# Performance work log

Hardware: AMD Instinct MI355X
Metric: run time of the kernel (lower is better)

The kernel has to match this reference:

```python
import jax, jax.numpy as jnp
import numpy as np


def setup_inputs() -> dict:
    key = jax.random.key(0)
    k1, k2, k3, k4 = jax.random.split(key, 4)
    B, T, E, H = 16, 2048, 1024, 128
    x = jax.random.normal(k1, (B, T, E), dtype=jnp.float32)
    Wk = jax.random.normal(k2, (E, H), dtype=jnp.float32) * (E ** -0.5)
    Wq = jax.random.normal(k3, (E, H), dtype=jnp.float32) * (E ** -0.5)
    Wv = jax.random.normal(k4, (E, H), dtype=jnp.float32) * (E ** -0.5)
    return {"x": x, "Wk": Wk, "Wq": Wq, "Wv": Wv}


def reference(x, Wk, Wq, Wv):
    # x: [B,T,E]; Wk/Wq/Wv: [E,H]
    B, T, E = x.shape
    H = Wk.shape[1]
    k = jnp.einsum('bte,eh->bth', x, Wk)
    q = jnp.einsum('bte,eh->bth', x, Wq)
    v = jnp.einsum('bte,eh->bth', x, Wv)
    # scores [B,T,T]; original masks with -inf THEN scales (equivalent math)
    scores = jnp.einsum('bqh,bkh->bqk', q, k) * (H ** -0.5)
    causal = jnp.tril(jnp.ones((T, T), dtype=bool))
    scores = jnp.where(causal, scores, -jnp.inf)
    weights = jax.nn.softmax(scores, axis=-1)
    # dropout disabled (eval mode reference)
    return jnp.einsum('bqk,bkh->bqh', weights, v)
```

## Files before the change

### kernel.cpp

```cpp
#include <hip/hip_runtime.h>

#define B_ 16
#define T_ 2048
#define E_ 1024
#define H_ 128

typedef short bf16x8 __attribute__((ext_vector_type(8)));
typedef float f32x4 __attribute__((ext_vector_type(4)));
typedef unsigned short u16x4 __attribute__((ext_vector_type(4)));

static __device__ __forceinline__ unsigned short f2bf(float f) {
    unsigned int u = __float_as_uint(f);
    u += 0x7FFFu + ((u >> 16) & 1u);
    return (unsigned short)(u >> 16);
}
static __device__ __forceinline__ unsigned int pk2(unsigned short a, unsigned short b) {
    return (unsigned int)a | ((unsigned int)b << 16);
}
static __device__ __forceinline__ bf16x8 frag(uint4 v) {
    return __builtin_bit_cast(bf16x8, v);
}

__global__ __launch_bounds__(256) void wcvt_kernel(
    const float* __restrict__ w0, const float* __restrict__ w1,
    const float* __restrict__ w2, unsigned short* __restrict__ wt)
{
    int g   = blockIdx.x * 256 + threadIdx.x;
    int arr = g >> 14;
    int rem = g & 16383;
    int h   = rem >> 7;
    int e0  = (rem & 127) * 8;
    const float* src = (arr == 0) ? w0 : (arr == 1) ? w1 : w2;
    unsigned short b[8];
#pragma unroll
    for (int i = 0; i < 8; i++) b[i] = f2bf(src[(size_t)(e0 + i) * H_ + h]);
    uint4 o;
    o.x = pk2(b[0], b[1]); o.y = pk2(b[2], b[3]);
    o.z = pk2(b[4], b[5]); o.w = pk2(b[6], b[7]);
    size_t off = ((size_t)(e0 >> 5) * 384 + arr * 128 + h) * 32 + (e0 & 31);
    *(uint4*)&wt[off] = o;
}

__global__ __launch_bounds__(384, 3) void proj_kernel(
    const float* __restrict__ x,
    const unsigned short* __restrict__ wt,
    unsigned short* __restrict__ q_ws,
    unsigned short* __restrict__ k_ws,
    unsigned short* __restrict__ vt_ws)
{
    const int m0    = blockIdx.x * 128;
    const int nbase = blockIdx.y * 192;
    __shared__ __align__(16) unsigned short Xs[128][40];
    __shared__ __align__(16) unsigned short Wl[192][40];

    const int tid  = threadIdx.x;
    const int lane = tid & 63;
    const int w    = tid >> 6;
    const int quad = lane >> 4;
    const int lm   = lane & 15;
    const int rw   = (w & 1) * 64;
    const int cw   = (w >> 1) * 64;

    const f32x4 z4 = {0.f, 0.f, 0.f, 0.f};
    f32x4 acc[4][4];
#pragma unroll
    for (int i = 0; i < 4; i++)
#pragma unroll
        for (int j = 0; j < 4; j++) acc[i][j] = z4;

    for (int kb = 0; kb < 32; kb++) {
        const int k0 = kb * 32;
        __syncthreads();
#pragma unroll
        for (int j = 0; j < 2; j++) {
            int idx = j * 384 + tid;
            if (idx < 512) {
                int row = idx >> 2, c = (idx & 3) * 8;
                const float* xp = x + (size_t)(m0 + row) * E_ + k0 + c;
                float4 a = *(const float4*)xp;
                float4 b = *(const float4*)(xp + 4);
                uint4 u;
                u.x = pk2(f2bf(a.x), f2bf(a.y));
                u.y = pk2(f2bf(a.z), f2bf(a.w));
                u.z = pk2(f2bf(b.x), f2bf(b.y));
                u.w = pk2(f2bf(b.z), f2bf(b.w));
                *(uint4*)&Xs[row][c] = u;
            }
        }
#pragma unroll
        for (int j = 0; j < 2; j++) {
            int fl = (j * 384 + tid) * 8;
            int nl = fl >> 5, kk = fl & 31;
            *(uint4*)&Wl[nl][kk] =
                *(const uint4*)&wt[((size_t)kb * 384 + nbase + nl) * 32 + kk];
        }
        __syncthreads();

        bf16x8 a[4], b[4];
#pragma unroll
        for (int am = 0; am < 4; am++)
            a[am] = frag(*(const uint4*)&Xs[rw + am * 16 + lm][quad * 8]);
#pragma unroll
        for (int bn = 0; bn < 4; bn++)
            b[bn] = frag(*(const uint4*)&Wl[cw + bn * 16 + lm][quad * 8]);
#pragma unroll
        for (int am = 0; am < 4; am++)
#pragma unroll
            for (int bn = 0; bn < 4; bn++)
                acc[am][bn] = __builtin_amdgcn_mfma_f32_16x16x32_bf16(
                    a[am], b[bn], acc[am][bn], 0, 0, 0);
    }

    const int bb = m0 >> 11;
    const int t0 = m0 & 2047;
#pragma unroll
    for (int am = 0; am < 4; am++)
#pragma unroll
        for (int bn = 0; bn < 4; bn++) {
            const int cg  = nbase + cw + bn * 16 + lm;
            const int row = m0 + rw + am * 16 + quad * 4;
            if (cg < 128) {
#pragma unroll
                for (int r = 0; r < 4; r++)
                    q_ws[(size_t)(row + r) * H_ + cg] = f2bf(acc[am][bn][r]);
            } else if (cg < 256) {
#pragma unroll
                for (int r = 0; r < 4; r++)
                    k_ws[(size_t)(row + r) * H_ + (cg - 128)] = f2bf(acc[am][bn][r]);
            } else {
                const int h  = cg - 256;
                const int tt = t0 + rw + am * 16 + quad * 4;
                u16x4 p;
#pragma unroll
                for (int r = 0; r < 4; r++) p[r] = f2bf(acc[am][bn][r]);
                *(u16x4*)&vt_ws[((size_t)(bb * 64 + (tt >> 5)) * 128 + h) * 32 + (tt & 31)] = p;
            }
        }
}

__global__ __launch_bounds__(128, 2) void attn_kernel(
    const unsigned short* __restrict__ q_ws,
    const unsigned short* __restrict__ k_ws,
    const unsigned short* __restrict__ vt_ws,
    float* __restrict__ out)
{
    const int batch = blockIdx.x & 15;
    const int pair  = blockIdx.x >> 4;

    __shared__ __align__(16) unsigned short Ps[2][16][40];
    __shared__ __align__(16) float Cb[64][40];

    const int tid  = threadIdx.x;
    const int lane = tid & 63;
    const int w    = tid >> 6;
    const int quad = lane >> 4;
    const int lm   = lane & 15;
    const float scale = 0.08838834764831845f;

    const size_t bq = (size_t)batch * T_ * H_;

    bf16x8 ones;
#pragma unroll
    for (int i = 0; i < 8; i++) ones[i] = (short)0x3F80;

    for (int half = 0; half < 2; half++) {
        const int t   = half ? (127 - pair) : pair;
        const int nkt = (t + 2) >> 1;

        bf16x8 qf[4];
#pragma unroll
        for (int h = 0; h < 4; h++)
            qf[h] = frag(*(const uint4*)(q_ws + bq +
                     (size_t)(t * 16 + lm) * H_ + h * 32 + quad * 8));

        const f32x4 z4 = {0.f, 0.f, 0.f, 0.f};
        f32x4 o[9];
#pragma unroll
        for (int f = 0; f < 9; f++) o[f] = z4;

        for (int kt = w; kt < nkt; kt += 2) {
            const int k0 = kt * 32;
            uint4 kr[2][4];
#pragma unroll
            for (int hf = 0; hf < 2; hf++)
#pragma unroll
                for (int h = 0; h < 4; h++)
                    kr[hf][h] = *(const uint4*)(k_ws + bq +
                        (size_t)(k0 + hf * 16 + lm) * H_ + h * 32 + quad * 8);
            uint4 vr[8];
#pragma unroll
            for (int f = 0; f < 8; f++)
                vr[f] = *(const uint4*)(vt_ws +
                    ((size_t)(batch * 64 + kt) * 128 + f * 16 + lm) * 32 + quad * 8);

            f32x4 st0 = z4, st1 = z4;
#pragma unroll
            for (int h = 0; h < 4; h++) {
                st0 = __builtin_amdgcn_mfma_f32_16x16x32_bf16(frag(kr[0][h]), qf[h], st0, 0, 0, 0);
                st1 = __builtin_amdgcn_mfma_f32_16x16x32_bf16(frag(kr[1][h]), qf[h], st1, 0, 0, 0);
            }
            const int qg = t * 16 + lm;
            u16x4 pa, pb;
#pragma unroll
            for (int r = 0; r < 4; r++) {
                int kv0 = k0 + quad * 4 + r;
                float e0 = __expf(st0[r] * scale);
                float e1 = __expf(st1[r] * scale);
                pa[r] = (kv0      <= qg) ? f2bf(e0) : (unsigned short)0;
                pb[r] = (kv0 + 16 <= qg) ? f2bf(e1) : (unsigned short)0;
            }
            *(u16x4*)&Ps[w][lm][quad * 4]      = pa;
            *(u16x4*)&Ps[w][lm][16 + quad * 4] = pb;
            bf16x8 pf = frag(*(const uint4*)&Ps[w][lm][quad * 8]);

#pragma unroll
            for (int f = 0; f < 8; f++)
                o[f] = __builtin_amdgcn_mfma_f32_16x16x32_bf16(pf, frag(vr[f]), o[f], 0, 0, 0);
            o[8] = __builtin_amdgcn_mfma_f32_16x16x32_bf16(pf, ones, o[8], 0, 0, 0);
        }

        __syncthreads();
        if (w == 1) {
#pragma unroll
            for (int f = 0; f < 9; f++) *(f32x4*)&Cb[lane][f * 4] = o[f];
        }
        __syncthreads();
        if (w == 0) {
#pragma unroll
            for (int f = 0; f < 9; f++) {
                f32x4 p = *(const f32x4*)&Cb[lane][f * 4];
                o[f] += p;
            }
            float* op = out + bq + (size_t)(t * 16) * H_;
#pragma unroll
            for (int r = 0; r < 4; r++) {
                float inv = 1.f / o[8][r];
#pragma unroll
                for (int f = 0; f < 8; f++)
                    op[(size_t)(quad * 4 + r) * H_ + f * 16 + lm] = o[f][r] * inv;
            }
        }
        __syncthreads();
    }
}

extern "C" void kernel_launch(void* const* d_in, const int* in_sizes, int n_in,
                              void* d_out, int out_size, void* d_ws, size_t ws_size,
                              hipStream_t stream)
{
    const float* x  = (const float*)d_in[0];
    const float* Wk = (const float*)d_in[1];
    const float* Wq = (const float*)d_in[2];
    const float* Wv = (const float*)d_in[3];
    float* out = (float*)d_out;

    const size_t MH = (size_t)B_ * T_ * H_;
    unsigned short* q_ws  = (unsigned short*)d_ws;
    unsigned short* k_ws  = q_ws + MH;
    unsigned short* vt_ws = k_ws + MH;
    unsigned short* wt    = vt_ws + MH;

    wcvt_kernel<<<dim3(192), dim3(256), 0, stream>>>(Wq, Wk, Wv, wt);
    proj_kernel<<<dim3(256, 2), dim3(384), 0, stream>>>(x, wt, q_ws, k_ws, vt_ws);
    attn_kernel<<<dim3(1024), dim3(128), 0, stream>>>(q_ws, k_ws, vt_ws, out);
}
```

Baseline: 333.8 us.

## Pre-convert x to bf16, prefetch projection tiles, widen attention to four waves

Adds a separate kernel that converts x to bf16 in workspace, so the projection kernel loads bf16 rows with register prefetch of the next k-slice instead of converting fp32 in the loop. The projection grid changes to 3 column blocks of 128 with 256 threads, and the weight layout becomes row-major per output column. The attention kernel goes from two waves to four per block, splitting key tiles four ways with a three-way reduction in shared memory. The extra full pass over x (read fp32, write bf16) adds memory traffic and may cost more than the conversion work it removes from the projection kernel.

```diff
diff --git a/kernel.cpp b/kernel.cpp
--- a/kernel.cpp
+++ b/kernel.cpp
@@ -19,6 +19,20 @@
 }
 static __device__ __forceinline__ bf16x8 frag(uint4 v) {
     return __builtin_bit_cast(bf16x8, v);
+}
+
+__global__ __launch_bounds__(256) void xcvt_kernel(
+    const float* __restrict__ x, unsigned short* __restrict__ xb)
+{
+    size_t i = ((size_t)blockIdx.x * 256 + threadIdx.x) * 8;
+    float4 a = *(const float4*)(x + i);
+    float4 b = *(const float4*)(x + i + 4);
+    uint4 o;
+    o.x = pk2(f2bf(a.x), f2bf(a.y));
+    o.y = pk2(f2bf(a.z), f2bf(a.w));
+    o.z = pk2(f2bf(b.x), f2bf(b.y));
+    o.w = pk2(f2bf(b.z), f2bf(b.w));
+    *(uint4*)(xb + i) = o;
 }
 
 __global__ __launch_bounds__(256) void wcvt_kernel(
@@ -37,21 +51,20 @@
     uint4 o;
     o.x = pk2(b[0], b[1]); o.y = pk2(b[2], b[3]);
     o.z = pk2(b[4], b[5]); o.w = pk2(b[6], b[7]);
-    size_t off = ((size_t)(e0 >> 5) * 384 + arr * 128 + h) * 32 + (e0 & 31);
-    *(uint4*)&wt[off] = o;
-}
-
-__global__ __launch_bounds__(384, 3) void proj_kernel(
-    const float* __restrict__ x,
+    *(uint4*)&wt[(size_t)(arr * 128 + h) * E_ + e0] = o;
+}
+
+__global__ __launch_bounds__(256, 2) void proj_kernel(
+    const unsigned short* __restrict__ xb,
     const unsigned short* __restrict__ wt,
     unsigned short* __restrict__ q_ws,
     unsigned short* __restrict__ k_ws,
     unsigned short* __restrict__ vt_ws)
 {
-    const int m0    = blockIdx.x * 128;
-    const int nbase = blockIdx.y * 192;
-    __shared__ __align__(16) unsigned short Xs[128][40];
-    __shared__ __align__(16) unsigned short Wl[192][40];
+    const int m0 = blockIdx.x * 128;
+    const int by = blockIdx.y;
+    __shared__ __align__(16) unsigned short As[128 * 32];
+    __shared__ __align__(16) unsigned short Bs[128 * 32];
 
     const int tid  = threadIdx.x;
     const int lane = tid & 63;
@@ -61,6 +74,11 @@
     const int rw   = (w & 1) * 64;
     const int cw   = (w >> 1) * 64;
 
+    const int r0 = tid >> 2;
+    const int kc = (tid & 3) * 8;
+    const unsigned short* xrow = xb + (size_t)(m0 + r0) * E_ + kc;
+    const unsigned short* wrow = wt + (size_t)(by * 128 + r0) * E_ + kc;
+
     const f32x4 z4 = {0.f, 0.f, 0.f, 0.f};
     f32x4 acc[4][4];
 #pragma unroll
@@ -68,41 +86,32 @@
 #pragma unroll
         for (int j = 0; j < 4; j++) acc[i][j] = z4;
 
+    uint4 pa0 = *(const uint4*)(xrow);
+    uint4 pa1 = *(const uint4*)(xrow + (size_t)64 * E_);
+    uint4 pb0 = *(const uint4*)(wrow);
+    uint4 pb1 = *(const uint4*)(wrow + (size_t)64 * E_);
+
     for (int kb = 0; kb < 32; kb++) {
-        const int k0 = kb * 32;
-        __syncthreads();
-#pragma unroll
-        for (int j = 0; j < 2; j++) {
-            int idx = j * 384 + tid;
-            if (idx < 512) {
-                int row = idx >> 2, c = (idx & 3) * 8;
-                const float* xp = x + (size_t)(m0 + row) * E_ + k0 + c;
-                float4 a = *(const float4*)xp;
-                float4 b = *(const float4*)(xp + 4);
-                uint4 u;
-                u.x = pk2(f2bf(a.x), f2bf(a.y));
-                u.y = pk2(f2bf(a.z), f2bf(a.w));
-                u.z = pk2(f2bf(b.x), f2bf(b.y));
-                u.w = pk2(f2bf(b.z), f2bf(b.w));
-                *(uint4*)&Xs[row][c] = u;
-            }
-        }
-#pragma unroll
-        for (int j = 0; j < 2; j++) {
-            int fl = (j * 384 + tid) * 8;
-            int nl = fl >> 5, kk = fl & 31;
-            *(uint4*)&Wl[nl][kk] =
-                *(const uint4*)&wt[((size_t)kb * 384 + nbase + nl) * 32 + kk];
-        }
-        __syncthreads();
+        __syncthreads();
+        *(uint4*)&As[tid * 8]          = pa0;
+        *(uint4*)&As[(tid + 256) * 8]  = pa1;
+        *(uint4*)&Bs[tid * 8]          = pb0;
+        *(uint4*)&Bs[(tid + 256) * 8]  = pb1;
+        __syncthreads();
+
+        const int kn = (kb < 31) ? (kb + 1) * 32 : 0;
+        pa0 = *(const uint4*)(xrow + kn);
+        pa1 = *(const uint4*)(xrow + (size_t)64 * E_ + kn);
+        pb0 = *(const uint4*)(wrow + kn);
+        pb1 = *(const uint4*)(wrow + (size_t)64 * E_ + kn);
 
         bf16x8 a[4], b[4];
 #pragma unroll
         for (int am = 0; am < 4; am++)
-            a[am] = frag(*(const uint4*)&Xs[rw + am * 16 + lm][quad * 8]);
+            a[am] = frag(*(const uint4*)&As[(rw + am * 16 + lm) * 32 + quad * 8]);
 #pragma unroll
         for (int bn = 0; bn < 4; bn++)
-            b[bn] = frag(*(const uint4*)&Wl[cw + bn * 16 + lm][quad * 8]);
+            b[bn] = frag(*(const uint4*)&Bs[(cw + bn * 16 + lm) * 32 + quad * 8]);
 #pragma unroll
         for (int am = 0; am < 4; am++)
 #pragma unroll
@@ -117,28 +126,27 @@
     for (int am = 0; am < 4; am++)
 #pragma unroll
         for (int bn = 0; bn < 4; bn++) {
-            const int cg  = nbase + cw + bn * 16 + lm;
+            const int col = cw + bn * 16 + lm;
             const int row = m0 + rw + am * 16 + quad * 4;
-            if (cg < 128) {
+            if (by == 0) {
 #pragma unroll
                 for (int r = 0; r < 4; r++)
-                    q_ws[(size_t)(row + r) * H_ + cg] = f2bf(acc[am][bn][r]);
-            } else if (cg < 256) {
+                    q_ws[(size_t)(row + r) * H_ + col] = f2bf(acc[am][bn][r]);
+            } else if (by == 1) {
 #pragma unroll
                 for (int r = 0; r < 4; r++)
-                    k_ws[(size_t)(row + r) * H_ + (cg - 128)] = f2bf(acc[am][bn][r]);
+                    k_ws[(size_t)(row + r) * H_ + col] = f2bf(acc[am][bn][r]);
             } else {
-                const int h  = cg - 256;
                 const int tt = t0 + rw + am * 16 + quad * 4;
                 u16x4 p;
 #pragma unroll
                 for (int r = 0; r < 4; r++) p[r] = f2bf(acc[am][bn][r]);
-                *(u16x4*)&vt_ws[((size_t)(bb * 64 + (tt >> 5)) * 128 + h) * 32 + (tt & 31)] = p;
-            }
-        }
-}
-
-__global__ __launch_bounds__(128, 2) void attn_kernel(
+                *(u16x4*)&vt_ws[((size_t)(bb * 64 + (tt >> 5)) * 128 + col) * 32 + (tt & 31)] = p;
+            }
+        }
+}
+
+__global__ __launch_bounds__(256, 3) void attn_kernel(
     const unsigned short* __restrict__ q_ws,
     const unsigned short* __restrict__ k_ws,
     const unsigned short* __restrict__ vt_ws,
@@ -147,12 +155,12 @@
     const int batch = blockIdx.x & 15;
     const int pair  = blockIdx.x >> 4;
 
-    __shared__ __align__(16) unsigned short Ps[2][16][40];
-    __shared__ __align__(16) float Cb[64][40];
+    __shared__ __align__(16) unsigned short Ps[4][16][40];
+    __shared__ __align__(16) float Cb[3][64][40];
 
     const int tid  = threadIdx.x;
     const int lane = tid & 63;
-    const int w    = tid >> 6;
+    const int ww   = tid >> 6;
     const int quad = lane >> 4;
     const int lm   = lane & 15;
     const float scale = 0.08838834764831845f;
@@ -163,6 +171,8 @@
 #pragma unroll
     for (int i = 0; i < 8; i++) ones[i] = (short)0x3F80;
 
+    const f32x4 z4 = {0.f, 0.f, 0.f, 0.f};
+
     for (int half = 0; half < 2; half++) {
         const int t   = half ? (127 - pair) : pair;
         const int nkt = (t + 2) >> 1;
@@ -173,13 +183,13 @@
             qf[h] = frag(*(const uint4*)(q_ws + bq +
                      (size_t)(t * 16 + lm) * H_ + h * 32 + quad * 8));
 
-        const f32x4 z4 = {0.f, 0.f, 0.f, 0.f};
         f32x4 o[9];
 #pragma unroll
         for (int f = 0; f < 9; f++) o[f] = z4;
 
-        for (int kt = w; kt < nkt; kt += 2) {
+        for (int kt = ww; kt < nkt; kt += 4) {
             const int k0 = kt * 32;
+
             uint4 kr[2][4];
 #pragma unroll
             for (int hf = 0; hf < 2; hf++)
@@ -187,18 +197,20 @@
                 for (int h = 0; h < 4; h++)
                     kr[hf][h] = *(const uint4*)(k_ws + bq +
                         (size_t)(k0 + hf * 16 + lm) * H_ + h * 32 + quad * 8);
+
+            f32x4 st0 = z4, st1 = z4;
+#pragma unroll
+            for (int h = 0; h < 4; h++) {
+                st0 = __builtin_amdgcn_mfma_f32_16x16x32_bf16(frag(kr[0][h]), qf[h], st0, 0, 0, 0);
+                st1 = __builtin_amdgcn_mfma_f32_16x16x32_bf16(frag(kr[1][h]), qf[h], st1, 0, 0, 0);
+            }
+
             uint4 vr[8];
 #pragma unroll
             for (int f = 0; f < 8; f++)
                 vr[f] = *(const uint4*)(vt_ws +
                     ((size_t)(batch * 64 + kt) * 128 + f * 16 + lm) * 32 + quad * 8);
 
-            f32x4 st0 = z4, st1 = z4;
-#pragma unroll
-            for (int h = 0; h < 4; h++) {
-                st0 = __builtin_amdgcn_mfma_f32_16x16x32_bf16(frag(kr[0][h]), qf[h], st0, 0, 0, 0);
-                st1 = __builtin_amdgcn_mfma_f32_16x16x32_bf16(frag(kr[1][h]), qf[h], st1, 0, 0, 0);
-            }
             const int qg = t * 16 + lm;
             u16x4 pa, pb;
 #pragma unroll
@@ -209,9 +221,9 @@
                 pa[r] = (kv0      <= qg) ? f2bf(e0) : (unsigned short)0;
                 pb[r] = (kv0 + 16 <= qg) ? f2bf(e1) : (unsigned short)0;
             }
-            *(u16x4*)&Ps[w][lm][quad * 4]      = pa;
-            *(u16x4*)&Ps[w][lm][16 + quad * 4] = pb;
-            bf16x8 pf = frag(*(const uint4*)&Ps[w][lm][quad * 8]);
+            *(u16x4*)&Ps[ww][lm][quad * 4]      = pa;
+            *(u16x4*)&Ps[ww][lm][16 + quad * 4] = pb;
+            bf16x8 pf = frag(*(const uint4*)&Ps[ww][lm][quad * 8]);
 
 #pragma unroll
             for (int f = 0; f < 8; f++)
@@ -220,17 +232,17 @@
         }
 
         __syncthreads();
-        if (w == 1) {
-#pragma unroll
-            for (int f = 0; f < 9; f++) *(f32x4*)&Cb[lane][f * 4] = o[f];
-        }
-        __syncthreads();
-        if (w == 0) {
-#pragma unroll
-            for (int f = 0; f < 9; f++) {
-                f32x4 p = *(const f32x4*)&Cb[lane][f * 4];
-                o[f] += p;
-            }
+        if (ww) {
+#pragma unroll
+            for (int f = 0; f < 9; f++) *(f32x4*)&Cb[ww - 1][lane][f * 4] = o[f];
+        }
+        __syncthreads();
+        if (!ww) {
+#pragma unroll
+            for (int s = 0; s < 3; s++)
+#pragma unroll
+                for (int f = 0; f < 9; f++)
+                    o[f] += *(const f32x4*)&Cb[s][lane][f * 4];
             float* op = out + bq + (size_t)(t * 16) * H_;
 #pragma unroll
             for (int r = 0; r < 4; r++) {
@@ -255,12 +267,15 @@
     float* out = (float*)d_out;
 
     const size_t MH = (size_t)B_ * T_ * H_;
+    const size_t ME = (size_t)B_ * T_ * E_;
     unsigned short* q_ws  = (unsigned short*)d_ws;
     unsigned short* k_ws  = q_ws + MH;
     unsigned short* vt_ws = k_ws + MH;
     unsigned short* wt    = vt_ws + MH;
-
+    unsigned short* xb    = wt + (size_t)384 * E_;
+
+    xcvt_kernel<<<dim3(ME / 2048), dim3(256), 0, stream>>>(x, xb);
     wcvt_kernel<<<dim3(192), dim3(256), 0, stream>>>(Wq, Wk, Wv, wt);
-    proj_kernel<<<dim3(256, 2), dim3(384), 0, stream>>>(x, wt, q_ws, k_ws, vt_ws);
-    attn_kernel<<<dim3(1024), dim3(128), 0, stream>>>(q_ws, k_ws, vt_ws, out);
-}
+    proj_kernel<<<dim3(256, 3), dim3(256), 0, stream>>>(xb, wt, q_ws, k_ws, vt_ws);
+    attn_kernel<<<dim3(1024), dim3(256), 0, stream>>>(q_ws, k_ws, vt_ws, out);
+}
```

New measurement: 336.3 us. About the same (+0.7%).
